# Optimization experiments

Hardware: AMD Instinct MI355X
Metric: run time of the kernel (lower is better)

Reference implementation:

```python
import jax, jax.numpy as jnp
import numpy as np

BETA = 1.0
G_MAX = 2.0
DECAY_RATE = 0.05
RECOVERY_RATE = 0.1
U_MIN, U_MAX = 0.01, 0.2


def setup_inputs() -> dict:
    key = jax.random.key(0)
    k1, _ = jax.random.split(key)
    B = 1048576
    u_initial = jax.random.uniform(k1, (B,), dtype=jnp.float32)  # unemployment in [0,1)
    u_trigger = jnp.float32(0.06)  # learnable threshold parameter
    return {"u_initial": u_initial, "u_trigger": u_trigger, "steps": 256}


def reference(u_initial, u_trigger, steps):
    def step(u, _):
        g = G_MAX * jax.nn.sigmoid(BETA * (u - u_trigger))
        u_next = jnp.clip(u + (DECAY_RATE - RECOVERY_RATE * g), U_MIN, U_MAX)
        return u_next, (u_next, g)

    _, (u_hist, g_hist) = jax.lax.scan(step, u_initial, None, length=steps)
    # u_hist, g_hist: [steps, B]
    return u_hist, g_hist
```

## Files before the change

kernel.cpp:

```cpp
#include <hip/hip_runtime.h>


#define VEC 4

__global__ __launch_bounds__(256) void stimulus_kernel(
    const float* __restrict__ u_init,
    const float* __restrict__ ut_p,
    float* __restrict__ u_hist,
    float* __restrict__ g_hist,
    int B, int steps)
{
    const int tid = blockIdx.x * blockDim.x + threadIdx.x;
    const size_t base = (size_t)tid * VEC;
    if (base >= (size_t)B) return;

    const float ut = ut_p[0];

    float4 in = *(const float4*)(u_init + base);
    float u[VEC] = {in.x, in.y, in.z, in.w};
    float g[VEC] = {0.f, 0.f, 0.f, 0.f};

    float* up = u_hist + base;
    float* gp = g_hist + base;

    int t = 0;

    for (; t < steps; ++t) {
        bool conv = true;
        #pragma unroll
        for (int j = 0; j < VEC; ++j) {
            float e = __expf(ut - u[j]);
            g[j] = 2.0f / (1.0f + e);
            float un = u[j] + (0.05f - 0.1f * g[j]);
            un = fminf(fmaxf(un, 0.01f), 0.2f);
            conv = conv && (un == u[j]);
            u[j] = un;
        }
        *(float4*)up = make_float4(u[0], u[1], u[2], u[3]);
        *(float4*)gp = make_float4(g[0], g[1], g[2], g[3]);
        up += B;
        gp += B;
        if (__all(conv)) { ++t; break; }
    }

    const float4 uc = make_float4(u[0], u[1], u[2], u[3]);
    const float4 gc = make_float4(g[0], g[1], g[2], g[3]);
    #pragma unroll 4
    for (; t < steps; ++t) {
        *(float4*)up = uc;
        *(float4*)gp = gc;
        up += B;
        gp += B;
    }
}

extern "C" void kernel_launch(void* const* d_in, const int* in_sizes, int n_in,
                              void* d_out, int out_size, void* d_ws, size_t ws_size,
                              hipStream_t stream) {
    const float* u_init = (const float*)d_in[0];
    const float* ut     = (const float*)d_in[1];
    const int B = in_sizes[0];
    const int steps = out_size / (2 * B);

    float* u_hist = (float*)d_out;
    float* g_hist = u_hist + (size_t)steps * (size_t)B;

    const int threads = (B + VEC - 1) / VEC;
    const int block = 256;
    const int grid = (threads + block - 1) / block;
    hipLaunchKernelGGL(stimulus_kernel, dim3(grid), dim3(block), 0, stream,
                       u_init, ut, u_hist, g_hist, B, steps);
}
```

Baseline: 2.220 ms.

## Bound convergence step analytically and fill converged tail with grid-stride stores

Each thread simulates the worst-case trajectory (starting at the upper clip 0.2) to find a step count S after which every element must sit at the 0.01 clamp. Per-element simulation is limited to the first S steps. The remaining rows are written as constant 0.01 and g(0.01) using a contiguous grid-stride store loop. This replaces the per-wave convergence detection and per-thread strided tail writes with one uniform, more streaming-friendly fill, aimed at raising write bandwidth on a store-bound kernel. It relies on the map being monotone and on the fixed point being the lower clamp; the bound search is recomputed redundantly in every thread.

```diff
diff --git a/kernel.cpp b/kernel.cpp
--- a/kernel.cpp
+++ b/kernel.cpp
@@ -2,6 +2,13 @@
 
 
 #define VEC 4
+
+__device__ __forceinline__ float step_u(float u, float ut, float& g) {
+    float e = __expf(ut - u);
+    g = 2.0f / (1.0f + e);
+    float un = u + (0.05f - 0.1f * g);
+    return fminf(fmaxf(un, 0.01f), 0.2f);
+}
 
 __global__ __launch_bounds__(256) void stimulus_kernel(
     const float* __restrict__ u_init,
@@ -11,46 +18,61 @@
     int B, int steps)
 {
     const int tid = blockIdx.x * blockDim.x + threadIdx.x;
-    const size_t base = (size_t)tid * VEC;
-    if (base >= (size_t)B) return;
-
+    const int nthreads = gridDim.x * blockDim.x;
     const float ut = ut_p[0];
 
-    float4 in = *(const float4*)(u_init + base);
-    float u[VEC] = {in.x, in.y, in.z, in.w};
-    float g[VEC] = {0.f, 0.f, 0.f, 0.f};
-
-    float* up = u_hist + base;
-    float* gp = g_hist + base;
-
-    int t = 0;
-
-    for (; t < steps; ++t) {
-        bool conv = true;
-        #pragma unroll
-        for (int j = 0; j < VEC; ++j) {
-            float e = __expf(ut - u[j]);
-            g[j] = 2.0f / (1.0f + e);
-            float un = u[j] + (0.05f - 0.1f * g[j]);
-            un = fminf(fmaxf(un, 0.01f), 0.2f);
-            conv = conv && (un == u[j]);
-            u[j] = un;
+    int S = steps;
+    {
+        float v = 0.2f;
+        for (int k = 1; k < steps; ++k) {
+            if (v <= 0.05f) { S = k + 2; break; }
+            float gd; v = step_u(v, ut, gd);
         }
-        *(float4*)up = make_float4(u[0], u[1], u[2], u[3]);
-        *(float4*)gp = make_float4(g[0], g[1], g[2], g[3]);
-        up += B;
-        gp += B;
-        if (__all(conv)) { ++t; break; }
+        if (S > steps) S = steps;
     }
 
-    const float4 uc = make_float4(u[0], u[1], u[2], u[3]);
-    const float4 gc = make_float4(g[0], g[1], g[2], g[3]);
-    #pragma unroll 4
-    for (; t < steps; ++t) {
-        *(float4*)up = uc;
-        *(float4*)gp = gc;
-        up += B;
-        gp += B;
+    const size_t base = (size_t)tid * VEC;
+    if (base < (size_t)B) {
+        float4 in = *(const float4*)(u_init + base);
+        float u[VEC] = {in.x, in.y, in.z, in.w};
+        float g[VEC] = {0.f, 0.f, 0.f, 0.f};
+        float* up = u_hist + base;
+        float* gp = g_hist + base;
+        int t = 0;
+        for (; t < S; ++t) {
+            bool conv = true;
+            #pragma unroll
+            for (int j = 0; j < VEC; ++j) {
+                float un = step_u(u[j], ut, g[j]);
+                conv = conv && (un == u[j]);
+                u[j] = un;
+            }
+            *(float4*)up = make_float4(u[0], u[1], u[2], u[3]);
+            *(float4*)gp = make_float4(g[0], g[1], g[2], g[3]);
+            up += B; gp += B;
+            if (S == steps && __all(conv)) { ++t; break; }
+        }
+        if (t < S) {
+            const float4 uc = make_float4(u[0], u[1], u[2], u[3]);
+            const float4 gc = make_float4(g[0], g[1], g[2], g[3]);
+            for (; t < S; ++t) {
+                *(float4*)up = uc;
+                *(float4*)gp = gc;
+                up += B; gp += B;
+            }
+        }
+    }
+
+    if (S < steps) {
+        float gk;
+        step_u(0.01f, ut, gk);
+        const size_t n4 = (size_t)(steps - S) * (size_t)(B / 4);
+        float4* ub = (float4*)(u_hist + (size_t)S * (size_t)B);
+        float4* gb = (float4*)(g_hist + (size_t)S * (size_t)B);
+        const float4 uc4 = make_float4(0.01f, 0.01f, 0.01f, 0.01f);
+        const float4 gc4 = make_float4(gk, gk, gk, gk);
+        for (size_t i = (size_t)tid; i < n4; i += (size_t)nthreads) ub[i] = uc4;
+        for (size_t i = (size_t)tid; i < n4; i += (size_t)nthreads) gb[i] = gc4;
     }
 }
 
```

After: 2.165 ms. -2.5%, faster.
